# Kernel optimization log

Measured on AMD Instinct MI355X. Metric: run time of the kernel, lower is better.

The kernel has to match this reference:

```python
import jax, jax.numpy as jnp
import numpy as np

B, T, I, H, C, S = 512, 128, 512, 512, 97, 26  # batch, enc_len, input, hidden, classes, num_steps


def setup_inputs() -> dict:
    key = jax.random.key(0)
    ks = jax.random.split(key, 12)
    s = 0.05
    d = {}
    d["batch_H"] = jax.random.normal(ks[0], (B, T, I), dtype=jnp.float32)
    d["text"] = jax.random.randint(ks[1], (B, S), 0, C)
    # attention cell params
    d["W_feat"] = jax.random.normal(ks[2], (H, I), dtype=jnp.float32) * s   # feature_projection (no bias)
    d["W_hid"] = jax.random.normal(ks[3], (H, H), dtype=jnp.float32) * s    # hidden_projection
    d["b_hid"] = jnp.zeros((H,), dtype=jnp.float32)
    d["w_score"] = jax.random.normal(ks[4], (H,), dtype=jnp.float32) * s    # attention_score (Linear(H,1), no bias)
    # LSTMCell params, PyTorch gate order [i, f, g, o]
    d["W_ih"] = jax.random.normal(ks[5], (4 * H, I + C), dtype=jnp.float32) * s
    d["W_hh"] = jax.random.normal(ks[6], (4 * H, H), dtype=jnp.float32) * s
    d["b_ih"] = jnp.zeros((4 * H,), dtype=jnp.float32)
    d["b_hh"] = jnp.zeros((4 * H,), dtype=jnp.float32)
    # generator
    d["W_gen"] = jax.random.normal(ks[7], (C, H), dtype=jnp.float32) * s
    d["b_gen"] = jnp.zeros((C,), dtype=jnp.float32)
    return d


def reference(batch_H, text, W_feat, W_hid, b_hid, w_score, W_ih, W_hh, b_ih, b_hh, W_gen, b_gen):
    Bb, Tt, _ = batch_H.shape
    Hh = W_hid.shape[0]
    Cc = W_gen.shape[0]
    # step-invariant: project encoder features once  [B, T, H]
    feat = jnp.einsum('bti,hi->bth', batch_H, W_feat)
    onehots = jax.nn.one_hot(text, Cc, dtype=batch_H.dtype)  # [B, S, C]

    def step(carry, oh):
        h, c = carry
        hp = h @ W_hid.T + b_hid                                     # [B, H]
        e = jnp.einsum('bth,h->bt', jnp.tanh(feat + hp[:, None, :]), w_score)
        alpha = jax.nn.softmax(e, axis=1)                            # [B, T]
        ctx = jnp.einsum('bt,bti->bi', alpha, batch_H)               # [B, I]
        x = jnp.concatenate([ctx, oh], axis=1)                       # [B, I+C]
        gates = x @ W_ih.T + b_ih + h @ W_hh.T + b_hh                # [B, 4H]
        i_g, f_g, g_g, o_g = jnp.split(gates, 4, axis=1)
        c2 = jax.nn.sigmoid(f_g) * c + jax.nn.sigmoid(i_g) * jnp.tanh(g_g)
        h2 = jax.nn.sigmoid(o_g) * jnp.tanh(c2)
        return (h2, c2), h2

    init = (jnp.zeros((Bb, Hh), dtype=batch_H.dtype), jnp.zeros((Bb, Hh), dtype=batch_H.dtype))
    _, hs = jax.lax.scan(step, init, jnp.swapaxes(onehots, 0, 1))    # hs: [S, B, H]
    out_h = jnp.swapaxes(hs, 0, 1)                                   # [B, S, H]
    probs = out_h @ W_gen.T + b_gen                                  # [B, S, C]
    return probs
```

## Files before the change

kernel.cpp:

```cpp
#include <hip/hip_runtime.h>
#include <hip/hip_bf16.h>
#include <stdint.h>
#include <stddef.h>

typedef __bf16 bf16;
typedef __bf16 v8bf __attribute__((ext_vector_type(8)));
typedef float  v4f  __attribute__((ext_vector_type(4)));

#define B_ 512
#define T_ 128
#define I_ 512
#define H_ 512
#define C_ 97
#define S_ 26

__device__ __forceinline__ void async_copy16(void* lds, const void* g) {
  __builtin_amdgcn_global_load_lds((__attribute__((address_space(1))) void*)g,
                                   (__attribute__((address_space(3))) void*)lds,
                                   16, 0, 0);
}

__device__ __forceinline__ float fast_tanh(float x) {
  float e = __expf(2.0f * x);
  return fmaf(-2.0f, __builtin_amdgcn_rcpf(e + 1.0f), 1.0f);
}
__device__ __forceinline__ float fast_sigmoid(float x) {
  float t = __expf(-x);
  return __builtin_amdgcn_rcpf(1.0f + t);
}

__device__ __forceinline__ void zero_acc(v4f acc[4][4]) {
  v4f z = {0.f, 0.f, 0.f, 0.f};
#pragma unroll
  for (int i = 0; i < 4; ++i)
#pragma unroll
    for (int j = 0; j < 4; ++j) acc[i][j] = z;
}

#define WAITBAR(N)                                             \
  do {                                                         \
    asm volatile("s_waitcnt vmcnt(" #N ")" ::: "memory");      \
    __builtin_amdgcn_s_barrier();                              \
    __builtin_amdgcn_sched_barrier(0);                         \
  } while (0)

template <int KTOT>
__device__ __forceinline__ void mm_qb32(const bf16* aRow0, const bf16* aRow1,
                                        const bf16* bRow0, const bf16* bRow1,
                                        bf16* As, bf16* Bs, int tid,
                                        v4f acc[4][4]) {
  constexpr int NT = KTOT / 32;
  const int wave = tid >> 6, lane = tid & 63;
  const int wr = (wave >> 1) * 64, wc = (wave & 1) * 64;
  const int fr = lane & 15, fq = lane >> 4;
  const int s0 = tid * 8;
  const int aB = (wr + fr) * 32 + fq * 8;
  const int bB = (wc + fr) * 32 + fq * 8;
#define STG32(bi, kk)                                   \
  do {                                                  \
    const int o = (bi) * 4096 + s0;                     \
    async_copy16(As + o, aRow0 + (kk));                 \
    async_copy16(As + o + 2048, aRow1 + (kk));          \
    async_copy16(Bs + o, bRow0 + (kk));                 \
    async_copy16(Bs + o + 2048, bRow1 + (kk));          \
  } while (0)
  STG32(0, 0);
  STG32(1, 32);
  for (int t = 0; t < NT; ++t) {
    if (t + 2 < NT) {
      STG32((t + 2) & 3, (t + 2) * 32);
      WAITBAR(8);
    } else if (t + 1 < NT) {
      WAITBAR(4);
    } else {
      WAITBAR(0);
    }
    const int cb = (t & 3) * 4096;
    v8bf av[4], bv[4];
#pragma unroll
    for (int i = 0; i < 4; ++i) av[i] = *(const v8bf*)(As + cb + aB + i * 512);
#pragma unroll
    for (int j = 0; j < 4; ++j) bv[j] = *(const v8bf*)(Bs + cb + bB + j * 512);
#pragma unroll
    for (int i = 0; i < 4; ++i) {
#pragma unroll
      for (int j = 0; j < 4; ++j) {
        acc[i][j] = __builtin_amdgcn_mfma_f32_16x16x32_bf16(av[i], bv[j], acc[i][j], 0, 0, 0);
      }
    }
  }
#undef STG32
}

template <int KTOT>
__device__ __forceinline__ void mm_reg_f32a(const float* aR0, const float* aR1,
                                            const bf16* bRow0, const bf16* bRow1,
                                            bf16* As, bf16* Bs, int tid,
                                            v4f acc[4][4]) {
  const int wave = tid >> 6, lane = tid & 63;
  const int wr = (wave >> 1) * 64, wc = (wave & 1) * 64;
  const int fr = lane & 15, fq = lane >> 4;
  bf16* a_s0 = As + tid * 8;
  bf16* a_s1 = As + (tid + 256) * 8;
  bf16* b_s0 = Bs + tid * 8;
  bf16* b_s1 = Bs + (tid + 256) * 8;
  const bf16* aF[4];
  const bf16* bF[4];
#pragma unroll
  for (int i = 0; i < 4; ++i) {
    aF[i] = As + (wr + i * 16 + fr) * 32 + fq * 8;
    bF[i] = Bs + (wc + i * 16 + fr) * 32 + fq * 8;
  }
  for (int kk = 0; kk < KTOT; kk += 32) {
    v8bf va0, va1;
    const float* p0 = aR0 + kk;
    const float* p1 = aR1 + kk;
    v4f f00 = ((const v4f*)p0)[0], f01 = ((const v4f*)p0)[1];
    v4f f10 = ((const v4f*)p1)[0], f11 = ((const v4f*)p1)[1];
#pragma unroll
    for (int j = 0; j < 4; ++j) {
      va0[j] = (bf16)f00[j]; va0[j + 4] = (bf16)f01[j];
      va1[j] = (bf16)f10[j]; va1[j + 4] = (bf16)f11[j];
    }
    v8bf vb0 = *(const v8bf*)(bRow0 + kk);
    v8bf vb1 = *(const v8bf*)(bRow1 + kk);
    __syncthreads();
    *(v8bf*)a_s0 = va0;
    *(v8bf*)a_s1 = va1;
    *(v8bf*)b_s0 = vb0;
    *(v8bf*)b_s1 = vb1;
    __syncthreads();
    v8bf av[4], bv[4];
#pragma unroll
    for (int i = 0; i < 4; ++i) av[i] = *(const v8bf*)aF[i];
#pragma unroll
    for (int j = 0; j < 4; ++j) bv[j] = *(const v8bf*)bF[j];
#pragma unroll
    for (int i = 0; i < 4; ++i) {
#pragma unroll
      for (int j = 0; j < 4; ++j) {
        acc[i][j] = __builtin_amdgcn_mfma_f32_16x16x32_bf16(av[i], bv[j], acc[i][j], 0, 0, 0);
      }
    }
  }
  __syncthreads();
}

__global__ void k_cvt(const float* __restrict__ src, bf16* __restrict__ dst, int n) {
  int i = (blockIdx.x * 256 + threadIdx.x) * 4;
  if (i + 3 < n) {
    v4f f = *(const v4f*)(src + i);
#pragma unroll
    for (int j = 0; j < 4; ++j) dst[i + j] = (bf16)f[j];
  }
}

__global__ void k_repack(const float* __restrict__ Wih, const float* __restrict__ Whh,
                         bf16* __restrict__ Wcat) {
  int n = blockIdx.x;
  int t = threadIdx.x;
#pragma unroll
  for (int j = 0; j < 4; ++j) {
    int k = t * 4 + j;
    float v = (k < 512) ? Wih[(size_t)n * 609 + k] : Whh[(size_t)n * 512 + (k - 512)];
    Wcat[(size_t)n * 1024 + k] = (bf16)v;
  }
}

__global__ void k_prep_gen(const float* __restrict__ Wg, bf16* __restrict__ Wgen16) {
  int row = blockIdx.x;
  int t = threadIdx.x;
#pragma unroll
  for (int j = 0; j < 2; ++j) {
    int k = t * 2 + j;
    float v = (row < C_) ? Wg[(size_t)row * 512 + k] : 0.0f;
    Wgen16[(size_t)row * 512 + k] = (bf16)v;
  }
}

__global__ void k_prep_oht(const float* __restrict__ Wih, float* __restrict__ OHT) {
  int n = blockIdx.x * 256 + threadIdx.x;
  const float* src = Wih + (size_t)n * 609 + 512;
  for (int c = 0; c < C_; ++c) OHT[(size_t)c * 2048 + n] = src[c];
}


__global__ __launch_bounds__(256, 2) void k_feat16(const bf16* __restrict__ A,
                                                   const bf16* __restrict__ Bw,
                                                   bf16* __restrict__ F) {
  __shared__ bf16 As[4 * 4096];
  __shared__ bf16 Bs[4 * 4096];
  const int tid = threadIdx.x;
  const int m0 = blockIdx.x * 128, n0 = blockIdx.y * 128;
  const int r0 = tid >> 2, k0 = (tid & 3) * 8;
  const bf16* aRow0 = A + (size_t)(m0 + r0) * 512 + k0;
  const bf16* aRow1 = A + (size_t)(m0 + r0 + 64) * 512 + k0;
  const bf16* bRow0 = Bw + (size_t)(n0 + r0) * 512 + k0;
  const bf16* bRow1 = Bw + (size_t)(n0 + r0 + 64) * 512 + k0;
  v4f acc[4][4];
  zero_acc(acc);
  mm_qb32<512>(aRow0, aRow1, bRow0, bRow1, As, Bs, tid, acc);
  const int wave = tid >> 6, lane = tid & 63;
  const int wr = (wave >> 1) * 64, wc = (wave & 1) * 64;
  const int fr = lane & 15, fq = lane >> 4;
#pragma unroll
  for (int i = 0; i < 4; ++i) {
#pragma unroll
    for (int j = 0; j < 4; ++j) {
      int col = n0 + wc + j * 16 + fr;
#pragma unroll
      for (int r = 0; r < 4; ++r) {
        int row = m0 + wr + i * 16 + fq * 4 + r;
        F[(size_t)row * 512 + col] = (bf16)acc[i][j][r];
      }
    }
  }
}

__global__ __launch_bounds__(256, 2) void k_feat32(const float* __restrict__ A,
                                                   const bf16* __restrict__ Bw,
                                                   bf16* __restrict__ F) {
  __shared__ bf16 As[128 * 32];
  __shared__ bf16 Bs[128 * 32];
  const int tid = threadIdx.x;
  const int m0 = blockIdx.x * 128, n0 = blockIdx.y * 128;
  const int r0 = tid >> 2, k0 = (tid & 3) * 8;
  const float* aRow0 = A + (size_t)(m0 + r0) * 512 + k0;
  const float* aRow1 = A + (size_t)(m0 + r0 + 64) * 512 + k0;
  const bf16* bRow0 = Bw + (size_t)(n0 + r0) * 512 + k0;
  const bf16* bRow1 = Bw + (size_t)(n0 + r0 + 64) * 512 + k0;
  v4f acc[4][4];
  zero_acc(acc);
  mm_reg_f32a<512>(aRow0, aRow1, bRow0, bRow1, As, Bs, tid, acc);
  const int wave = tid >> 6, lane = tid & 63;
  const int wr = (wave >> 1) * 64, wc = (wave & 1) * 64;
  const int fr = lane & 15, fq = lane >> 4;
#pragma unroll
  for (int i = 0; i < 4; ++i) {
#pragma unroll
    for (int j = 0; j < 4; ++j) {
      int col = n0 + wc + j * 16 + fr;
#pragma unroll
      for (int r = 0; r < 4; ++r) {
        int row = m0 + wr + i * 16 + fq * 4 + r;
        F[(size_t)row * 512 + col] = (bf16)acc[i][j][r];
      }
    }
  }
}

__global__ __launch_bounds__(256) void k_hp(const bf16* __restrict__ xb_cur,
                                            const bf16* __restrict__ Whid16,
                                            const float* __restrict__ b_hid,
                                            float* __restrict__ P) {
  __shared__ bf16 As[4 * 4096];
  __shared__ bf16 Bs[4 * 4096];
  const int tid = threadIdx.x, wave = tid >> 6, lane = tid & 63;
  const int m0 = blockIdx.x * 64, n0 = blockIdx.y * 64;
  const int r0 = tid >> 2, k0 = (tid & 3) * 8;
  const bf16* aRow = xb_cur + (size_t)(m0 + r0) * 1024 + 512 + k0;
  const bf16* bRow = Whid16 + (size_t)(n0 + r0) * 512 + k0;
  const int s0 = tid * 8;
  const int fr = lane & 15, fq = lane >> 4;
  const int aB = fr * 32 + fq * 8;
  const int bB = (wave * 16 + fr) * 32 + fq * 8;
  v4f acc[4];
  v4f z = {0.f, 0.f, 0.f, 0.f};
#pragma unroll
  for (int i = 0; i < 4; ++i) acc[i] = z;
#define STGH(bi, kk)                                    \
  do {                                                  \
    const int o = (bi) * 4096 + s0;                     \
    async_copy16(As + o, aRow + (kk));                  \
    async_copy16(As + o + 2048, aRow + (kk) + 32);      \
    async_copy16(Bs + o, bRow + (kk));                  \
    async_copy16(Bs + o + 2048, bRow + (kk) + 32);      \
  } while (0)
  STGH(0, 0);
  STGH(1, 64);
  constexpr int NT = 8;
  for (int t = 0; t < NT; ++t) {
    if (t + 2 < NT) {
      STGH((t + 2) & 3, (t + 2) * 64);
      WAITBAR(8);
    } else if (t + 1 < NT) {
      WAITBAR(4);
    } else {
      WAITBAR(0);
    }
    const int cb = (t & 3) * 4096;
#pragma unroll
    for (int ks = 0; ks < 2; ++ks) {
      const int sb = cb + ks * 2048;
      v8bf bv = *(const v8bf*)(Bs + sb + bB);
#pragma unroll
      for (int i = 0; i < 4; ++i) {
        acc[i] = __builtin_amdgcn_mfma_f32_16x16x32_bf16(*(const v8bf*)(As + sb + aB + i * 512),
                                                         bv, acc[i], 0, 0, 0);
      }
    }
  }
#undef STGH
  const int col = n0 + wave * 16 + fr;
  const float bh = b_hid[col];
#pragma unroll
  for (int i = 0; i < 4; ++i) {
#pragma unroll
    for (int r = 0; r < 4; ++r) {
      int row = m0 + i * 16 + fq * 4 + r;
      P[(size_t)row * 512 + col] = acc[i][r] + bh;
    }
  }
}

template <bool CTX16>
__global__ __launch_bounds__(512, 4) void k_attn(const bf16* __restrict__ F,
                                                 const float* __restrict__ P,
                                                 const float* __restrict__ w_score,
                                                 const void* __restrict__ bHv,
                                                 bf16* __restrict__ xb_cur) {
  const int b = blockIdx.x;
  const int tid = threadIdx.x, wave = tid >> 6, lane = tid & 63;
  __shared__ float e_s[T_];
  __shared__ float alpha_s[T_];
  __shared__ float red[8][I_];
  float Pv[8], Wv[8];
  {
    const float* p = P + (size_t)b * H_ + lane * 8;
#pragma unroll
    for (int j = 0; j < 8; ++j) Pv[j] = p[j];
    const float* w = w_score + lane * 8;
#pragma unroll
    for (int j = 0; j < 8; ++j) Wv[j] = w[j];
  }
  const bf16* Fb = F + (size_t)b * T_ * H_ + lane * 8;
#pragma unroll
  for (int t = wave; t < T_; t += 32) {
    v8bf r0 = *(const v8bf*)(Fb + (size_t)t * H_);
    v8bf r1 = *(const v8bf*)(Fb + (size_t)(t + 8) * H_);
    v8bf r2 = *(const v8bf*)(Fb + (size_t)(t + 16) * H_);
    v8bf r3 = *(const v8bf*)(Fb + (size_t)(t + 24) * H_);
    float a0 = 0.f, a1 = 0.f, a2 = 0.f, a3 = 0.f;
#pragma unroll
    for (int j = 0; j < 8; ++j) a0 = fmaf(Wv[j], fast_tanh((float)r0[j] + Pv[j]), a0);
#pragma unroll
    for (int j = 0; j < 8; ++j) a1 = fmaf(Wv[j], fast_tanh((float)r1[j] + Pv[j]), a1);
#pragma unroll
    for (int j = 0; j < 8; ++j) a2 = fmaf(Wv[j], fast_tanh((float)r2[j] + Pv[j]), a2);
#pragma unroll
    for (int j = 0; j < 8; ++j) a3 = fmaf(Wv[j], fast_tanh((float)r3[j] + Pv[j]), a3);
#pragma unroll
    for (int off = 32; off; off >>= 1) {
      a0 += __shfl_xor(a0, off, 64);
      a1 += __shfl_xor(a1, off, 64);
      a2 += __shfl_xor(a2, off, 64);
      a3 += __shfl_xor(a3, off, 64);
    }
    if (lane == 0) {
      e_s[t] = a0; e_s[t + 8] = a1; e_s[t + 16] = a2; e_s[t + 24] = a3;
    }
  }
  __syncthreads();
  if (wave == 0) {
    float e0 = e_s[lane], e1 = e_s[lane + 64];
    float m = fmaxf(e0, e1);
#pragma unroll
    for (int off = 32; off; off >>= 1) m = fmaxf(m, __shfl_xor(m, off, 64));
    float x0 = __expf(e0 - m), x1 = __expf(e1 - m);
    float ssum = x0 + x1;
#pragma unroll
    for (int off = 32; off; off >>= 1) ssum += __shfl_xor(ssum, off, 64);
    float inv = __builtin_amdgcn_rcpf(ssum);
    alpha_s[lane] = x0 * inv;
    alpha_s[lane + 64] = x1 * inv;
  }
  __syncthreads();
  const int i0 = lane * 8;
  float c[8];
#pragma unroll
  for (int j = 0; j < 8; ++j) c[j] = 0.f;
  if (CTX16) {
    const bf16* hb = (const bf16*)bHv + (size_t)b * T_ * I_ + i0;
#pragma unroll
    for (int t = wave; t < T_; t += 32) {
      float aa0 = alpha_s[t], aa1 = alpha_s[t + 8];
      float aa2 = alpha_s[t + 16], aa3 = alpha_s[t + 24];
      v8bf p0 = *(const v8bf*)(hb + (size_t)t * I_);
      v8bf p1 = *(const v8bf*)(hb + (size_t)(t + 8) * I_);
      v8bf p2 = *(const v8bf*)(hb + (size_t)(t + 16) * I_);
      v8bf p3 = *(const v8bf*)(hb + (size_t)(t + 24) * I_);
#pragma unroll
      for (int j = 0; j < 8; ++j) {
        c[j] = fmaf(aa0, (float)p0[j], c[j]);
        c[j] = fmaf(aa1, (float)p1[j], c[j]);
        c[j] = fmaf(aa2, (float)p2[j], c[j]);
        c[j] = fmaf(aa3, (float)p3[j], c[j]);
      }
    }
  } else {
    const float* hf = (const float*)bHv + (size_t)b * T_ * I_ + i0;
#pragma unroll
    for (int t = wave; t < T_; t += 32) {
      float aa0 = alpha_s[t], aa1 = alpha_s[t + 8];
      float aa2 = alpha_s[t + 16], aa3 = alpha_s[t + 24];
      const float* p0 = hf + (size_t)t * I_;
      const float* p1 = hf + (size_t)(t + 8) * I_;
      const float* p2 = hf + (size_t)(t + 16) * I_;
      const float* p3 = hf + (size_t)(t + 24) * I_;
      v4f q00 = ((const v4f*)p0)[0], q01 = ((const v4f*)p0)[1];
      v4f q10 = ((const v4f*)p1)[0], q11 = ((const v4f*)p1)[1];
      v4f q20 = ((const v4f*)p2)[0], q21 = ((const v4f*)p2)[1];
      v4f q30 = ((const v4f*)p3)[0], q31 = ((const v4f*)p3)[1];
#pragma unroll
      for (int j = 0; j < 4; ++j) {
        c[j]     = fmaf(aa0, q00[j], c[j]);
        c[j + 4] = fmaf(aa0, q01[j], c[j + 4]);
        c[j]     = fmaf(aa1, q10[j], c[j]);
        c[j + 4] = fmaf(aa1, q11[j], c[j + 4]);
        c[j]     = fmaf(aa2, q20[j], c[j]);
        c[j + 4] = fmaf(aa2, q21[j], c[j + 4]);
        c[j]     = fmaf(aa3, q30[j], c[j]);
        c[j + 4] = fmaf(aa3, q31[j], c[j + 4]);
      }
    }
  }
#pragma unroll
  for (int j = 0; j < 8; ++j) red[wave][i0 + j] = c[j];
  __syncthreads();
  {
    int i = tid;
    float s = red[0][i] + red[1][i] + red[2][i] + red[3][i] +
              red[4][i] + red[5][i] + red[6][i] + red[7][i];
    xb_cur[(size_t)b * 1024 + i] = (bf16)s;
  }
}

__global__ __launch_bounds__(256) void k_gates(const bf16* __restrict__ xb_cur,
                                               const bf16* __restrict__ Wcat,
                                               const float* __restrict__ OHT,
                                               const float* __restrict__ b_ih,
                                               const float* __restrict__ b_hh,
                                               const int* __restrict__ text,
                                               float* __restrict__ c_state,
                                               bf16* __restrict__ out_h,
                                               bf16* __restrict__ xb_nxt, int s) {
  __shared__ union {
    struct { bf16 A[4 * 4096]; bf16 Bv[4 * 4096]; } st;
    float Cs[128 * 132];
  } sm;
  const int tid = threadIdx.x;
  const int m0 = blockIdx.x * 128;
  const int j0 = blockIdx.y * 32;
  const int r0 = tid >> 2, k0 = (tid & 3) * 8;
  const int nw0 = (r0 >> 5) * 512 + j0 + (r0 & 31);
  const int nw1 = (((r0 + 64) >> 5)) * 512 + j0 + ((r0 + 64) & 31);
  const bf16* aRow0 = xb_cur + (size_t)(m0 + r0) * 1024 + k0;
  const bf16* aRow1 = xb_cur + (size_t)(m0 + r0 + 64) * 1024 + k0;
  const bf16* bRow0 = Wcat + (size_t)nw0 * 1024 + k0;
  const bf16* bRow1 = Wcat + (size_t)nw1 * 1024 + k0;
  v4f acc[4][4];
  zero_acc(acc);
  mm_qb32<1024>(aRow0, aRow1, bRow0, bRow1, sm.st.A, sm.st.Bv, tid, acc);
  __syncthreads();
  const int wave = tid >> 6, lane = tid & 63;
  const int wr = (wave >> 1) * 64, wc = (wave & 1) * 64;
  const int fr = lane & 15, fq = lane >> 4;
  int tcv[4][4];
#pragma unroll
  for (int i = 0; i < 4; ++i) {
#pragma unroll
    for (int r = 0; r < 4; ++r) {
      tcv[i][r] = text[(size_t)(m0 + wr + i * 16 + fq * 4 + r) * S_ + s];
    }
  }
#pragma unroll
  for (int j = 0; j < 4; ++j) {
    int cl = wc + j * 16 + fr;
    int nw = (cl >> 5) * 512 + j0 + (cl & 31);
    float bias = b_ih[nw] + b_hh[nw];
    const float* oh = OHT + nw;
#pragma unroll
    for (int i = 0; i < 4; ++i) {
#pragma unroll
      for (int r = 0; r < 4; ++r) {
        int rl = wr + i * 16 + fq * 4 + r;
        sm.Cs[rl * 132 + cl] = acc[i][j][r] + bias + oh[(size_t)tcv[i][r] * 2048];
      }
    }
  }
  __syncthreads();
#pragma unroll
  for (int it = 0; it < 16; ++it) {
    int idx = tid + it * 256;
    int r = idx >> 5, q = idx & 31;
    float ig = sm.Cs[r * 132 + q];
    float fg = sm.Cs[r * 132 + 32 + q];
    float gg = sm.Cs[r * 132 + 64 + q];
    float og = sm.Cs[r * 132 + 96 + q];
    size_t cix = (size_t)(m0 + r) * 512 + j0 + q;
    float c2 = fast_sigmoid(fg) * c_state[cix] + fast_sigmoid(ig) * fast_tanh(gg);
    float h2 = fast_sigmoid(og) * fast_tanh(c2);
    c_state[cix] = c2;
    bf16 hb = (bf16)h2;
    xb_nxt[(size_t)(m0 + r) * 1024 + 512 + j0 + q] = hb;
    out_h[((size_t)(m0 + r) * S_ + s) * 512 + j0 + q] = hb;
  }
}

__global__ __launch_bounds__(256) void k_gen(const bf16* __restrict__ out_h,
                                             const bf16* __restrict__ Wgen16,
                                             const float* __restrict__ b_gen,
                                             float* __restrict__ out) {
  __shared__ bf16 As[4 * 4096];
  __shared__ bf16 Bs[4 * 4096];
  const int tid = threadIdx.x;
  const int m0 = blockIdx.x * 128;
  const int r0 = tid >> 2, k0 = (tid & 3) * 8;
  const bf16* aRow0 = out_h + (size_t)(m0 + r0) * 512 + k0;
  const bf16* aRow1 = out_h + (size_t)(m0 + r0 + 64) * 512 + k0;
  const bf16* bRow0 = Wgen16 + (size_t)r0 * 512 + k0;
  const bf16* bRow1 = Wgen16 + (size_t)(r0 + 64) * 512 + k0;
  v4f acc[4][4];
  zero_acc(acc);
  mm_qb32<512>(aRow0, aRow1, bRow0, bRow1, As, Bs, tid, acc);
  const int wave = tid >> 6, lane = tid & 63;
  const int wr = (wave >> 1) * 64, wc = (wave & 1) * 64;
  const int fr = lane & 15, fq = lane >> 4;
#pragma unroll
  for (int i = 0; i < 4; ++i) {
#pragma unroll
    for (int j = 0; j < 4; ++j) {
      int col = wc + j * 16 + fr;
      if (col < C_) {
        float bg = b_gen[col];
#pragma unroll
        for (int r = 0; r < 4; ++r) {
          int row = m0 + wr + i * 16 + fq * 4 + r;
          out[(size_t)row * C_ + col] = acc[i][j][r] + bg;
        }
      }
    }
  }
}

extern "C" void kernel_launch(void* const* d_in, const int* in_sizes, int n_in,
                              void* d_out, int out_size, void* d_ws, size_t ws_size,
                              hipStream_t stream) {
  (void)in_sizes; (void)n_in; (void)out_size;
  const float* batch_H = (const float*)d_in[0];
  const int*   text    = (const int*)d_in[1];
  const float* W_feat  = (const float*)d_in[2];
  const float* W_hid   = (const float*)d_in[3];
  const float* b_hid   = (const float*)d_in[4];
  const float* w_score = (const float*)d_in[5];
  const float* W_ih    = (const float*)d_in[6];
  const float* W_hh    = (const float*)d_in[7];
  const float* b_ih    = (const float*)d_in[8];
  const float* b_hh    = (const float*)d_in[9];
  const float* W_gen   = (const float*)d_in[10];
  const float* b_gen   = (const float*)d_in[11];
  float* out = (float*)d_out;

  char* ws = (char*)d_ws;
  bf16*  F       = (bf16*)(ws);
  bf16*  out_h   = (bf16*)(ws + 67108864);
  float* P       = (float*)(ws + 80740352);
  bf16*  xb0     = (bf16*)(ws + 81788928);
  bf16*  xb1     = (bf16*)(ws + 82837504);
  float* c_state = (float*)(ws + 83886080);
  bf16*  Wcat    = (bf16*)(ws + 84934656);
  bf16*  Wf16    = (bf16*)(ws + 89128960);
  bf16*  Whid16  = (bf16*)(ws + 89653248);
  bf16*  Wgen16  = (bf16*)(ws + 90177536);
  float* OHT     = (float*)(ws + 90308608);
  bf16*  bH16    = (bf16*)(ws + 91357184);
  const bool useBH16 = (ws_size >= (size_t)158466048);

  bf16* xb[2] = {xb0, xb1};

  hipMemsetAsync(xb0, 0, (size_t)512 * 1024 * 2, stream);
  hipMemsetAsync(c_state, 0, (size_t)512 * 512 * 4, stream);

  k_cvt<<<dim3(256), 256, 0, stream>>>(W_feat, Wf16, 512 * 512);
  k_cvt<<<dim3(256), 256, 0, stream>>>(W_hid, Whid16, 512 * 512);
  k_repack<<<dim3(2048), 256, 0, stream>>>(W_ih, W_hh, Wcat);
  k_prep_gen<<<dim3(128), 256, 0, stream>>>(W_gen, Wgen16);
  k_prep_oht<<<dim3(8), 256, 0, stream>>>(W_ih, OHT);

  if (useBH16) {
    k_cvt<<<dim3(32768), 256, 0, stream>>>(batch_H, bH16, B_ * T_ * I_);
    k_feat16<<<dim3(512, 4), 256, 0, stream>>>(bH16, Wf16, F);
  } else {
    k_feat32<<<dim3(512, 4), 256, 0, stream>>>(batch_H, Wf16, F);
  }

  for (int s = 0; s < S_; ++s) {
    bf16* cur = xb[s & 1];
    bf16* nxt = xb[(s + 1) & 1];
    k_hp<<<dim3(8, 8), 256, 0, stream>>>(cur, Whid16, b_hid, P);
    if (useBH16) {
      k_attn<true><<<dim3(512), 512, 0, stream>>>(F, P, w_score, bH16, cur);
    } else {
      k_attn<false><<<dim3(512), 512, 0, stream>>>(F, P, w_score, batch_H, cur);
    }
    k_gates<<<dim3(4, 16), 256, 0, stream>>>(cur, Wcat, OHT, b_ih, b_hh, text,
                                             c_state, out_h, nxt, s);
  }
  k_gen<<<dim3(104, 1), 256, 0, stream>>>(out_h, Wgen16, b_gen, out);
}
```

Before: 1.535 ms.

## Shrink per-step GEMM tiles, swizzle LDS, and simplify attention tanh/softmax

The hidden-projection and gate GEMMs inside the recurrent loop now use smaller M tiles (32 rows), so each step launches 128 and 256 blocks instead of 64 each and fills more CUs. Both GEMMs load full 64-wide K rows into LDS with an XOR swizzle to avoid bank conflicts. The attention kernel rewrites w·tanh(x) as sum(w) minus 2·w·sigmoid-style terms computed with a prescaled exp2, which saves a multiply per element. Every wave now computes the softmax redundantly and passes alpha through shuffles, which removes the alpha shared array and one barrier. Smaller tiles reload the weights more often and give less reuse per block.

```diff
diff --git a/kernel.cpp b/kernel.cpp
--- a/kernel.cpp
+++ b/kernel.cpp
@@ -253,28 +253,25 @@
                                             const bf16* __restrict__ Whid16,
                                             const float* __restrict__ b_hid,
                                             float* __restrict__ P) {
-  __shared__ bf16 As[4 * 4096];
+  __shared__ bf16 As[4 * 2048];
   __shared__ bf16 Bs[4 * 4096];
   const int tid = threadIdx.x, wave = tid >> 6, lane = tid & 63;
-  const int m0 = blockIdx.x * 64, n0 = blockIdx.y * 64;
-  const int r0 = tid >> 2, k0 = (tid & 3) * 8;
-  const bf16* aRow = xb_cur + (size_t)(m0 + r0) * 1024 + 512 + k0;
-  const bf16* bRow = Whid16 + (size_t)(n0 + r0) * 512 + k0;
+  const int m0 = blockIdx.x * 32, n0 = blockIdx.y * 64;
+  const int fr = lane & 15, fq = lane >> 4;
+  const int ra = tid >> 3, sa = (tid & 7) ^ (ra & 7);
+  const bf16* aSrc = xb_cur + (size_t)(m0 + ra) * 1024 + 512 + sa * 8;
+  const int rb0 = tid >> 3, rb1 = (tid >> 3) + 32;
+  const bf16* bSrc0 = Whid16 + (size_t)(n0 + rb0) * 512 + (((tid & 7) ^ (rb0 & 7)) * 8);
+  const bf16* bSrc1 = Whid16 + (size_t)(n0 + rb1) * 512 + (((tid & 7) ^ (rb1 & 7)) * 8);
   const int s0 = tid * 8;
-  const int fr = lane & 15, fq = lane >> 4;
-  const int aB = fr * 32 + fq * 8;
-  const int bB = (wave * 16 + fr) * 32 + fq * 8;
-  v4f acc[4];
+  v4f acc[2];
   v4f z = {0.f, 0.f, 0.f, 0.f};
-#pragma unroll
-  for (int i = 0; i < 4; ++i) acc[i] = z;
+  acc[0] = z; acc[1] = z;
 #define STGH(bi, kk)                                    \
   do {                                                  \
-    const int o = (bi) * 4096 + s0;                     \
-    async_copy16(As + o, aRow + (kk));                  \
-    async_copy16(As + o + 2048, aRow + (kk) + 32);      \
-    async_copy16(Bs + o, bRow + (kk));                  \
-    async_copy16(Bs + o + 2048, bRow + (kk) + 32);      \
+    async_copy16(As + (bi) * 2048 + s0, aSrc + (kk));   \
+    async_copy16(Bs + (bi) * 4096 + s0, bSrc0 + (kk));  \
+    async_copy16(Bs + (bi) * 4096 + 2048 + s0, bSrc1 + (kk)); \
   } while (0)
   STGH(0, 0);
   STGH(1, 64);
@@ -282,21 +279,22 @@
   for (int t = 0; t < NT; ++t) {
     if (t + 2 < NT) {
       STGH((t + 2) & 3, (t + 2) * 64);
-      WAITBAR(8);
+      WAITBAR(6);
     } else if (t + 1 < NT) {
-      WAITBAR(4);
+      WAITBAR(3);
     } else {
       WAITBAR(0);
     }
-    const int cb = (t & 3) * 4096;
+    const int cb4 = (t & 3) * 2048;
+    const int cb8 = (t & 3) * 4096;
 #pragma unroll
     for (int ks = 0; ks < 2; ++ks) {
-      const int sb = cb + ks * 2048;
-      v8bf bv = *(const v8bf*)(Bs + sb + bB);
-#pragma unroll
-      for (int i = 0; i < 4; ++i) {
-        acc[i] = __builtin_amdgcn_mfma_f32_16x16x32_bf16(*(const v8bf*)(As + sb + aB + i * 512),
-                                                         bv, acc[i], 0, 0, 0);
+      const int sw = ((ks * 4 + fq) ^ (fr & 7)) * 8;
+      v8bf bv = *(const v8bf*)(Bs + cb8 + (wave * 16 + fr) * 64 + sw);
+#pragma unroll
+      for (int i = 0; i < 2; ++i) {
+        v8bf av = *(const v8bf*)(As + cb4 + (i * 16 + fr) * 64 + sw);
+        acc[i] = __builtin_amdgcn_mfma_f32_16x16x32_bf16(av, bv, acc[i], 0, 0, 0);
       }
     }
   }
@@ -304,7 +302,7 @@
   const int col = n0 + wave * 16 + fr;
   const float bh = b_hid[col];
 #pragma unroll
-  for (int i = 0; i < 4; ++i) {
+  for (int i = 0; i < 2; ++i) {
 #pragma unroll
     for (int r = 0; r < 4; ++r) {
       int row = m0 + i * 16 + fq * 4 + r;
@@ -322,33 +320,43 @@
   const int b = blockIdx.x;
   const int tid = threadIdx.x, wave = tid >> 6, lane = tid & 63;
   __shared__ float e_s[T_];
-  __shared__ float alpha_s[T_];
   __shared__ float red[8][I_];
-  float Pv[8], Wv[8];
+  const float CF = 2.8853900817779268f;
+  float pl[8], Wv[8];
   {
     const float* p = P + (size_t)b * H_ + lane * 8;
 #pragma unroll
-    for (int j = 0; j < 8; ++j) Pv[j] = p[j];
+    for (int j = 0; j < 8; ++j) pl[j] = CF * p[j];
     const float* w = w_score + lane * 8;
 #pragma unroll
     for (int j = 0; j < 8; ++j) Wv[j] = w[j];
   }
+  float sW = 0.f;
+#pragma unroll
+  for (int j = 0; j < 8; ++j) sW += Wv[j];
+#pragma unroll
+  for (int off = 32; off; off >>= 1) sW += __shfl_xor(sW, off, 64);
   const bf16* Fb = F + (size_t)b * T_ * H_ + lane * 8;
 #pragma unroll
-  for (int t = wave; t < T_; t += 32) {
+  for (int k = 0; k < 4; ++k) {
+    const int t = wave + 32 * k;
     v8bf r0 = *(const v8bf*)(Fb + (size_t)t * H_);
     v8bf r1 = *(const v8bf*)(Fb + (size_t)(t + 8) * H_);
     v8bf r2 = *(const v8bf*)(Fb + (size_t)(t + 16) * H_);
     v8bf r3 = *(const v8bf*)(Fb + (size_t)(t + 24) * H_);
     float a0 = 0.f, a1 = 0.f, a2 = 0.f, a3 = 0.f;
 #pragma unroll
-    for (int j = 0; j < 8; ++j) a0 = fmaf(Wv[j], fast_tanh((float)r0[j] + Pv[j]), a0);
-#pragma unroll
-    for (int j = 0; j < 8; ++j) a1 = fmaf(Wv[j], fast_tanh((float)r1[j] + Pv[j]), a1);
-#pragma unroll
-    for (int j = 0; j < 8; ++j) a2 = fmaf(Wv[j], fast_tanh((float)r2[j] + Pv[j]), a2);
-#pragma unroll
-    for (int j = 0; j < 8; ++j) a3 = fmaf(Wv[j], fast_tanh((float)r3[j] + Pv[j]), a3);
+    for (int j = 0; j < 8; ++j)
+      a0 = fmaf(Wv[j], __builtin_amdgcn_rcpf(1.0f + exp2f(fmaf(CF, (float)r0[j], pl[j]))), a0);
+#pragma unroll
+    for (int j = 0; j < 8; ++j)
+      a1 = fmaf(Wv[j], __builtin_amdgcn_rcpf(1.0f + exp2f(fmaf(CF, (float)r1[j], pl[j]))), a1);
+#pragma unroll
+    for (int j = 0; j < 8; ++j)
+      a2 = fmaf(Wv[j], __builtin_amdgcn_rcpf(1.0f + exp2f(fmaf(CF, (float)r2[j], pl[j]))), a2);
+#pragma unroll
+    for (int j = 0; j < 8; ++j)
+      a3 = fmaf(Wv[j], __builtin_amdgcn_rcpf(1.0f + exp2f(fmaf(CF, (float)r3[j], pl[j]))), a3);
 #pragma unroll
     for (int off = 32; off; off >>= 1) {
       a0 += __shfl_xor(a0, off, 64);
@@ -357,24 +365,28 @@
       a3 += __shfl_xor(a3, off, 64);
     }
     if (lane == 0) {
-      e_s[t] = a0; e_s[t + 8] = a1; e_s[t + 16] = a2; e_s[t + 24] = a3;
+      e_s[t] = sW - 2.0f * a0;
+      e_s[t + 8] = sW - 2.0f * a1;
+      e_s[t + 16] = sW - 2.0f * a2;
+      e_s[t + 24] = sW - 2.0f * a3;
     }
   }
   __syncthreads();
-  if (wave == 0) {
+  float x0, x1;
+  {
     float e0 = e_s[lane], e1 = e_s[lane + 64];
     float m = fmaxf(e0, e1);
 #pragma unroll
     for (int off = 32; off; off >>= 1) m = fmaxf(m, __shfl_xor(m, off, 64));
-    float x0 = __expf(e0 - m), x1 = __expf(e1 - m);
+    x0 = __expf(e0 - m);
+    x1 = __expf(e1 - m);
     float ssum = x0 + x1;
 #pragma unroll
     for (int off = 32; off; off >>= 1) ssum += __shfl_xor(ssum, off, 64);
     float inv = __builtin_amdgcn_rcpf(ssum);
-    alpha_s[lane] = x0 * inv;
-    alpha_s[lane + 64] = x1 * inv;
-  }
-  __syncthreads();
+    x0 *= inv;
+    x1 *= inv;
+  }
   const int i0 = lane * 8;
   float c[8];
 #pragma unroll
@@ -382,9 +394,12 @@
   if (CTX16) {
     const bf16* hb = (const bf16*)bHv + (size_t)b * T_ * I_ + i0;
 #pragma unroll
-    for (int t = wave; t < T_; t += 32) {
-      float aa0 = alpha_s[t], aa1 = alpha_s[t + 8];
-      float aa2 = alpha_s[t + 16], aa3 = alpha_s[t + 24];
+    for (int k = 0; k < 4; ++k) {
+      const int t = wave + 32 * k;
+      float aa0 = __shfl(k < 2 ? x0 : x1, t & 63, 64);
+      float aa1 = __shfl(k < 2 ? x0 : x1, (t + 8) & 63, 64);
+      float aa2 = __shfl(k < 2 ? x0 : x1, (t + 16) & 63, 64);
+      float aa3 = __shfl(k < 2 ? x0 : x1, (t + 24) & 63, 64);
       v8bf p0 = *(const v8bf*)(hb + (size_t)t * I_);
       v8bf p1 = *(const v8bf*)(hb + (size_t)(t + 8) * I_);
       v8bf p2 = *(const v8bf*)(hb + (size_t)(t + 16) * I_);
@@ -400,9 +415,12 @@
   } else {
     const float* hf = (const float*)bHv + (size_t)b * T_ * I_ + i0;
 #pragma unroll
-    for (int t = wave; t < T_; t += 32) {
-      float aa0 = alpha_s[t], aa1 = alpha_s[t + 8];
-      float aa2 = alpha_s[t + 16], aa3 = alpha_s[t + 24];
+    for (int k = 0; k < 4; ++k) {
+      const int t = wave + 32 * k;
+      float aa0 = __shfl(k < 2 ? x0 : x1, t & 63, 64);
+      float aa1 = __shfl(k < 2 ? x0 : x1, (t + 8) & 63, 64);
+      float aa2 = __shfl(k < 2 ? x0 : x1, (t + 16) & 63, 64);
+      float aa3 = __shfl(k < 2 ? x0 : x1, (t + 24) & 63, 64);
       const float* p0 = hf + (size_t)t * I_;
       const float* p1 = hf + (size_t)(t + 8) * I_;
       const float* p2 = hf + (size_t)(t + 16) * I_;
@@ -445,52 +463,94 @@
                                                bf16* __restrict__ out_h,
                                                bf16* __restrict__ xb_nxt, int s) {
   __shared__ union {
-    struct { bf16 A[4 * 4096]; bf16 Bv[4 * 4096]; } st;
-    float Cs[128 * 132];
+    struct { bf16 A[4 * 2048]; bf16 Bv[4 * 8192]; } st;
+    float Cs[32 * 132];
   } sm;
   const int tid = threadIdx.x;
-  const int m0 = blockIdx.x * 128;
+  const int m0 = blockIdx.x * 32;
   const int j0 = blockIdx.y * 32;
-  const int r0 = tid >> 2, k0 = (tid & 3) * 8;
-  const int nw0 = (r0 >> 5) * 512 + j0 + (r0 & 31);
-  const int nw1 = (((r0 + 64) >> 5)) * 512 + j0 + ((r0 + 64) & 31);
-  const bf16* aRow0 = xb_cur + (size_t)(m0 + r0) * 1024 + k0;
-  const bf16* aRow1 = xb_cur + (size_t)(m0 + r0 + 64) * 1024 + k0;
-  const bf16* bRow0 = Wcat + (size_t)nw0 * 1024 + k0;
-  const bf16* bRow1 = Wcat + (size_t)nw1 * 1024 + k0;
-  v4f acc[4][4];
-  zero_acc(acc);
-  mm_qb32<1024>(aRow0, aRow1, bRow0, bRow1, sm.st.A, sm.st.Bv, tid, acc);
+  const int wave = tid >> 6, lane = tid & 63;
+  const int fr = lane & 15, fq = lane >> 4;
+  const int s0 = tid * 8;
+  const int ra = tid >> 3, sa = (tid & 7) ^ (ra & 7);
+  const bf16* aSrc = xb_cur + (size_t)(m0 + ra) * 1024 + sa * 8;
+  const bf16* bSrc[4];
+#pragma unroll
+  for (int cc = 0; cc < 4; ++cc) {
+    const int rb = (tid >> 3) + cc * 32;
+    const int nw = (rb >> 5) * 512 + j0 + (rb & 31);
+    bSrc[cc] = Wcat + (size_t)nw * 1024 + (((tid & 7) ^ (rb & 7)) * 8);
+  }
+  v4f acc[2][2];
+  {
+    v4f z = {0.f, 0.f, 0.f, 0.f};
+    acc[0][0] = z; acc[0][1] = z; acc[1][0] = z; acc[1][1] = z;
+  }
+#define STGG(bi, kk)                                                 \
+  do {                                                               \
+    async_copy16(sm.st.A + (bi) * 2048 + s0, aSrc + (kk));           \
+    async_copy16(sm.st.Bv + (bi) * 8192 + s0, bSrc[0] + (kk));       \
+    async_copy16(sm.st.Bv + (bi) * 8192 + 2048 + s0, bSrc[1] + (kk)); \
+    async_copy16(sm.st.Bv + (bi) * 8192 + 4096 + s0, bSrc[2] + (kk)); \
+    async_copy16(sm.st.Bv + (bi) * 8192 + 6144 + s0, bSrc[3] + (kk)); \
+  } while (0)
+  STGG(0, 0);
+  STGG(1, 64);
+  constexpr int NT = 16;
+  for (int t = 0; t < NT; ++t) {
+    if (t + 2 < NT) {
+      STGG((t + 2) & 3, (t + 2) * 64);
+      WAITBAR(10);
+    } else if (t + 1 < NT) {
+      WAITBAR(5);
+    } else {
+      WAITBAR(0);
+    }
+    const int ca = (t & 3) * 2048;
+    const int cbv = (t & 3) * 8192;
+#pragma unroll
+    for (int ks = 0; ks < 2; ++ks) {
+      const int sw = ((ks * 4 + fq) ^ (fr & 7)) * 8;
+      v8bf av[2], bv[2];
+#pragma unroll
+      for (int i = 0; i < 2; ++i)
+        av[i] = *(const v8bf*)(sm.st.A + ca + (i * 16 + fr) * 64 + sw);
+#pragma unroll
+      for (int jf = 0; jf < 2; ++jf)
+        bv[jf] = *(const v8bf*)(sm.st.Bv + cbv + (wave * 32 + jf * 16 + fr) * 64 + sw);
+#pragma unroll
+      for (int i = 0; i < 2; ++i)
+#pragma unroll
+        for (int jf = 0; jf < 2; ++jf)
+          acc[i][jf] = __builtin_amdgcn_mfma_f32_16x16x32_bf16(av[i], bv[jf], acc[i][jf], 0, 0, 0);
+    }
+  }
+#undef STGG
   __syncthreads();
-  const int wave = tid >> 6, lane = tid & 63;
-  const int wr = (wave >> 1) * 64, wc = (wave & 1) * 64;
-  const int fr = lane & 15, fq = lane >> 4;
-  int tcv[4][4];
-#pragma unroll
-  for (int i = 0; i < 4; ++i) {
-#pragma unroll
-    for (int r = 0; r < 4; ++r) {
-      tcv[i][r] = text[(size_t)(m0 + wr + i * 16 + fq * 4 + r) * S_ + s];
-    }
-  }
-#pragma unroll
-  for (int j = 0; j < 4; ++j) {
-    int cl = wc + j * 16 + fr;
+  int tcv[2][4];
+#pragma unroll
+  for (int i = 0; i < 2; ++i)
+#pragma unroll
+    for (int r = 0; r < 4; ++r)
+      tcv[i][r] = text[(size_t)(m0 + i * 16 + fq * 4 + r) * S_ + s];
+#pragma unroll
+  for (int jf = 0; jf < 2; ++jf) {
+    int cl = wave * 32 + jf * 16 + fr;
     int nw = (cl >> 5) * 512 + j0 + (cl & 31);
     float bias = b_ih[nw] + b_hh[nw];
     const float* oh = OHT + nw;
 #pragma unroll
-    for (int i = 0; i < 4; ++i) {
+    for (int i = 0; i < 2; ++i) {
 #pragma unroll
       for (int r = 0; r < 4; ++r) {
-        int rl = wr + i * 16 + fq * 4 + r;
-        sm.Cs[rl * 132 + cl] = acc[i][j][r] + bias + oh[(size_t)tcv[i][r] * 2048];
+        int rl = i * 16 + fq * 4 + r;
+        sm.Cs[rl * 132 + cl] = acc[i][jf][r] + bias + oh[(size_t)tcv[i][r] * 2048];
       }
     }
   }
   __syncthreads();
 #pragma unroll
-  for (int it = 0; it < 16; ++it) {
+  for (int it = 0; it < 4; ++it) {
     int idx = tid + it * 256;
     int r = idx >> 5, q = idx & 31;
     float ig = sm.Cs[r * 132 + q];
@@ -597,14 +657,14 @@
   for (int s = 0; s < S_; ++s) {
     bf16* cur = xb[s & 1];
     bf16* nxt = xb[(s + 1) & 1];
-    k_hp<<<dim3(8, 8), 256, 0, stream>>>(cur, Whid16, b_hid, P);
+    k_hp<<<dim3(16, 8), 256, 0, stream>>>(cur, Whid16, b_hid, P);
     if (useBH16) {
       k_attn<true><<<dim3(512), 512, 0, stream>>>(F, P, w_score, bH16, cur);
     } else {
       k_attn<false><<<dim3(512), 512, 0, stream>>>(F, P, w_score, batch_H, cur);
     }
-    k_gates<<<dim3(4, 16), 256, 0, stream>>>(cur, Wcat, OHT, b_ih, b_hh, text,
-                                             c_state, out_h, nxt, s);
+    k_gates<<<dim3(16, 16), 256, 0, stream>>>(cur, Wcat, OHT, b_ih, b_hh, text,
+                                              c_state, out_h, nxt, s);
   }
   k_gen<<<dim3(104, 1), 256, 0, stream>>>(out_h, Wgen16, b_gen, out);
 }
```

Result: faster. 1.447 ms (-5.7%).
